# Performance work log

Hardware: AMD Instinct MI355X
Metric: run time of the kernel (lower is better)

Reference implementation:

```python
import jax, jax.numpy as jnp
import numpy as np

N_HEADS = 16
D_EMBED = 1024
D_HEAD = D_EMBED // N_HEADS
CAUSAL = True


def setup_inputs() -> dict:
    key = jax.random.key(0)
    k1, k2, k3, k4, k5 = jax.random.split(key, 5)
    B, S = 2, 2048
    scale = 1.0 / np.sqrt(D_EMBED)
    return {
        "x": jax.random.normal(k1, (B, S, D_EMBED), dtype=jnp.float32),
        "Wqkv": jax.random.normal(k2, (D_EMBED, 3 * D_EMBED), dtype=jnp.float32) * scale,
        "bqkv": jax.random.normal(k3, (3 * D_EMBED,), dtype=jnp.float32) * 0.01,
        "Wo": jax.random.normal(k4, (D_EMBED, D_EMBED), dtype=jnp.float32) * scale,
        "bo": jax.random.normal(k5, (D_EMBED,), dtype=jnp.float32) * 0.01,
    }


def reference(x, Wqkv, bqkv, Wo, bo):
    B, S, D = x.shape
    qkv = x @ Wqkv + bqkv                      # [B,S,3D]
    q, k, v = jnp.split(qkv, 3, axis=-1)
    # [B,S,D] -> [B,H,S,dh]
    def heads(t):
        return t.reshape(B, S, N_HEADS, D_HEAD).transpose(0, 2, 1, 3)
    q, k, v = heads(q), heads(k), heads(v)
    scores = jnp.einsum('bhqd,bhkd->bhqk', q, k)
    if CAUSAL:
        mask = jnp.triu(jnp.ones((S, S), dtype=bool), k=1)  # True above diagonal
        scores = jnp.where(mask, -jnp.inf, scores)
    scores = scores / jnp.sqrt(jnp.asarray(D_HEAD, dtype=scores.dtype))
    attn = jax.nn.softmax(scores, axis=-1)
    out = jnp.einsum('bhqk,bhkd->bhqd', attn, v)           # [B,H,S,dh]
    out = out.transpose(0, 2, 1, 3).reshape(B, S, D)
    return out @ Wo + bo
```

## Files before the change

kernel.cpp:

```cpp
#include <hip/hip_runtime.h>
#include <hip/hip_bf16.h>
#include <cstdint>
#include <cstddef>


using bf16 = __hip_bfloat16;
typedef __attribute__((ext_vector_type(8))) short short8;
typedef __attribute__((ext_vector_type(4))) float f32x4;
typedef __attribute__((ext_vector_type(16))) float f32x16;
typedef __attribute__((ext_vector_type(4))) unsigned int u32x4;

__device__ __forceinline__ unsigned short f2b(float f) {
    bf16 h = __float2bfloat16(f);
    return *reinterpret_cast<unsigned short*>(&h);
}

__device__ __forceinline__ void async16(const void* g, void* l) {
    __builtin_amdgcn_global_load_lds(
        (const __attribute__((address_space(1))) void*)g,
        (__attribute__((address_space(3))) void*)l, 16, 0, 0);
}

__global__ __launch_bounds__(256) void cvt_kernel(const float* __restrict__ in,
                                                  bf16* __restrict__ out, int n4) {
    int i = blockIdx.x * 256 + threadIdx.x;
    if (i >= n4) return;
    const float4 v = reinterpret_cast<const float4*>(in)[i];
    ushort4 o;
    o.x = f2b(v.x); o.y = f2b(v.y); o.z = f2b(v.z); o.w = f2b(v.w);
    reinterpret_cast<ushort4*>(out)[i] = o;
}

__global__ __launch_bounds__(256) void transpose_cvt(const float* __restrict__ in,
                                                     bf16* __restrict__ out,
                                                     int K, int N) {
    __shared__ float tile[32][33];
    int n0 = blockIdx.x * 32, k0 = blockIdx.y * 32;
    int tx = threadIdx.x, ty = threadIdx.y;
    #pragma unroll
    for (int i = 0; i < 32; i += 8)
        tile[ty + i][tx] = in[(size_t)(k0 + ty + i) * N + n0 + tx];
    __syncthreads();
    #pragma unroll
    for (int i = 0; i < 32; i += 8)
        out[(size_t)(n0 + ty + i) * K + k0 + tx] = __float2bfloat16(tile[tx][ty + i]);
}

template <int EPI>
__global__ __launch_bounds__(256) void gemm_bt64(
    const bf16* __restrict__ A,
    const bf16* __restrict__ Bt,
    const float* __restrict__ bias,
    float* __restrict__ Cf,
    bf16* __restrict__ qd, bf16* __restrict__ kd, bf16* __restrict__ vtd,
    int M, int N, int K) {
    __shared__ bf16 As[128 * 64];
    __shared__ bf16 Bs[128 * 64];
    const int t = threadIdx.x;
    const int lane = t & 63;
    const int lr = lane & 15, lg = lane >> 4;
    const int wave = t >> 6;
    const int wr = wave >> 1, wc = wave & 1;
    const int m0 = blockIdx.x * 128, n0 = blockIdx.y * 128;

    const int sRow = t >> 3;
    const int sChunk = (t & 7) ^ (sRow & 7);
    const bf16* aSrc = A + (size_t)(m0 + sRow) * K + sChunk * 8;
    const bf16* bSrc = Bt + (size_t)(n0 + sRow) * K + sChunk * 8;
    const size_t rowStep32 = (size_t)32 * K;

    f32x4 acc[4][4] = {};

    for (int k0 = 0; k0 < K; k0 += 64) {
        __syncthreads();
        #pragma unroll
        for (int j = 0; j < 4; ++j) {
            async16(aSrc + j * rowStep32 + k0, &As[j * 2048 + t * 8]);
            async16(bSrc + j * rowStep32 + k0, &Bs[j * 2048 + t * 8]);
        }
        __syncthreads();
        #pragma unroll
        for (int kh = 0; kh < 2; ++kh) {
            short8 af[4], bfr[4];
            #pragma unroll
            for (int i = 0; i < 4; ++i) {
                const int ar = wr * 64 + i * 16 + lr;
                af[i] = *reinterpret_cast<const short8*>(
                    &As[ar * 64 + ((kh * 4 + lg) ^ (ar & 7)) * 8]);
                const int br = wc * 64 + i * 16 + lr;
                bfr[i] = *reinterpret_cast<const short8*>(
                    &Bs[br * 64 + ((kh * 4 + lg) ^ (br & 7)) * 8]);
            }
            #pragma unroll
            for (int mi = 0; mi < 4; ++mi)
                #pragma unroll
                for (int ni = 0; ni < 4; ++ni)
                    acc[mi][ni] = __builtin_amdgcn_mfma_f32_16x16x32_bf16(
                        af[mi], bfr[ni], acc[mi][ni], 0, 0, 0);
        }
    }

    #pragma unroll
    for (int mi = 0; mi < 4; ++mi) {
        #pragma unroll
        for (int ni = 0; ni < 4; ++ni) {
            #pragma unroll
            for (int r = 0; r < 4; ++r) {
                const int row = m0 + wr * 64 + mi * 16 + lg * 4 + r;
                const int col = n0 + wc * 64 + ni * 16 + lr;
                const float v = acc[mi][ni][r] + bias[col];
                if constexpr (EPI == 0) {
                    Cf[(size_t)row * N + col] = v;
                } else {
                    const bf16 hv = __float2bfloat16(v);
                    const int part = col >> 10;
                    const int within = col & 1023;
                    const int h = within >> 6, d = within & 63;
                    const int b = row >> 11, s = row & 2047;
                    const int bh = b * 16 + h;
                    if (part == 0)
                        qd[((size_t)bh * 2048 + s) * 64 + d] = hv;
                    else if (part == 1)
                        kd[((size_t)bh * 2048 + s) * 64 + d] = hv;
                    else
                        vtd[((size_t)bh * 64 + d) * 2048 + s] = hv;
                }
            }
        }
    }
}

__global__ __launch_bounds__(256, 2) void attn_kernel(const bf16* __restrict__ q,
                                                      const bf16* __restrict__ k,
                                                      const bf16* __restrict__ vt,
                                                      bf16* __restrict__ o) {
    const int S = 2048;
    const int f = blockIdx.x;
    const int res = f & 7, m = f >> 3;
    const int grp = m >> 4;
    const int bh = res + 8 * grp;
    const int bxr = m & 15;
    const int bx = (grp & 2) ? (15 - bxr) : bxr;
    const int b = bh >> 4, h = bh & 15;
    const int w = threadIdx.x >> 6;
    const int u = w >> 1, par = w & 1;
    const int lane = threadIdx.x & 63;
    const int ln = lane & 31;
    const int hi = lane >> 5;
    const int P = 2 * (15 - bx) + u;
    const int qbaseA = P * 64;
    const int qbaseB = P * 64 + 32;

    const bf16* qp = q + (size_t)bh * S * 64;
    const bf16* kp = k + (size_t)bh * S * 64;
    const bf16* vp = vt + (size_t)bh * 64 * S;

    short8 qfA[4], qfB[4];
    #pragma unroll
    for (int i = 0; i < 4; ++i) {
        qfA[i] = *reinterpret_cast<const short8*>(
            &qp[(size_t)(qbaseA + ln) * 64 + i * 16 + hi * 8]);
        qfB[i] = *reinterpret_cast<const short8*>(
            &qp[(size_t)(qbaseB + ln) * 64 + i * 16 + hi * 8]);
    }

    f32x16 oA0 = {}, oA1 = {}, oB0 = {}, oB1 = {};
    f32x4 lsvA = {0.f, 0.f, 0.f, 0.f}, lsvB = {0.f, 0.f, 0.f, 0.f};

    short8 kA[4], kB[4], vA[4], vB[4];

    auto kload = [&](short8 (&kf)[4], int tile) {
        const bf16* base = &kp[(size_t)(tile * 32 + ln) * 64 + hi * 8];
        #pragma unroll
        for (int i = 0; i < 4; ++i)
            kf[i] = *reinterpret_cast<const short8*>(base + i * 16);
    };
    auto vload = [&](short8 (&vf)[4], int tile) {
        #pragma unroll
        for (int dblk = 0; dblk < 2; ++dblk)
            #pragma unroll
            for (int half = 0; half < 2; ++half)
                vf[dblk * 2 + half] = *reinterpret_cast<const short8*>(
                    &vp[(size_t)(dblk * 32 + ln) * S + tile * 32 + half * 16 +
                        hi * 8]);
    };

    auto body = [&](const short8 (&kf)[4], const short8 (&vf)[4],
                    const short8 (&qf)[4], f32x16& o0, f32x16& o1, f32x4& lsv,
                    bool diag) {
        f32x16 z0 = {}, z1 = {};
        z0 = __builtin_amdgcn_mfma_f32_32x32x16_bf16(kf[0], qf[0], z0, 0, 0, 0);
        z0 = __builtin_amdgcn_mfma_f32_32x32x16_bf16(kf[1], qf[1], z0, 0, 0, 0);
        z1 = __builtin_amdgcn_mfma_f32_32x32x16_bf16(kf[2], qf[2], z1, 0, 0, 0);
        z1 = __builtin_amdgcn_mfma_f32_32x32x16_bf16(kf[3], qf[3], z1, 0, 0, 0);
        const f32x16 z = z0 + z1;
        f32x16 pv;
        #pragma unroll
        for (int r = 0; r < 16; ++r) {
            const int kreg = (r & 3) + 8 * (r >> 2) + 4 * hi;
            float e = __expf(z[r] * 0.125f);
            if (diag && (kreg > ln)) e = 0.f;
            pv[r] = e;
            lsv[r & 3] += e;
        }
        unsigned a0, a1, b0, b1, c0, c1, d0, d1;
        asm("v_cvt_pk_bf16_f32 %0, %1, %2" : "=v"(a0) : "v"(pv[0]), "v"(pv[1]));
        asm("v_cvt_pk_bf16_f32 %0, %1, %2" : "=v"(a1) : "v"(pv[2]), "v"(pv[3]));
        asm("v_cvt_pk_bf16_f32 %0, %1, %2" : "=v"(b0) : "v"(pv[4]), "v"(pv[5]));
        asm("v_cvt_pk_bf16_f32 %0, %1, %2" : "=v"(b1) : "v"(pv[6]), "v"(pv[7]));
        asm("v_cvt_pk_bf16_f32 %0, %1, %2" : "=v"(c0) : "v"(pv[8]), "v"(pv[9]));
        asm("v_cvt_pk_bf16_f32 %0, %1, %2" : "=v"(c1) : "v"(pv[10]), "v"(pv[11]));
        asm("v_cvt_pk_bf16_f32 %0, %1, %2" : "=v"(d0) : "v"(pv[12]), "v"(pv[13]));
        asm("v_cvt_pk_bf16_f32 %0, %1, %2" : "=v"(d1) : "v"(pv[14]), "v"(pv[15]));
        asm("v_permlane32_swap_b32 %0, %1" : "+v"(a0), "+v"(b0));
        asm("v_permlane32_swap_b32 %0, %1" : "+v"(a1), "+v"(b1));
        asm("v_permlane32_swap_b32 %0, %1" : "+v"(c0), "+v"(d0));
        asm("v_permlane32_swap_b32 %0, %1" : "+v"(c1), "+v"(d1));
        u32x4 t0, t1;
        t0[0] = a0; t0[1] = a1; t0[2] = b0; t0[3] = b1;
        t1[0] = c0; t1[1] = c1; t1[2] = d0; t1[3] = d1;
        const short8 pa0 = __builtin_bit_cast(short8, t0);
        const short8 pa1 = __builtin_bit_cast(short8, t1);
        o0 = __builtin_amdgcn_mfma_f32_32x32x16_bf16(pa0, vf[0], o0, 0, 0, 0);
        o0 = __builtin_amdgcn_mfma_f32_32x32x16_bf16(pa1, vf[1], o0, 0, 0, 0);
        o1 = __builtin_amdgcn_mfma_f32_32x32x16_bf16(pa0, vf[2], o1, 0, 0, 0);
        o1 = __builtin_amdgcn_mfma_f32_32x32x16_bf16(pa1, vf[3], o1, 0, 0, 0);
    };

    auto dual = [&](const short8 (&kf)[4], const short8 (&vf)[4]) {
        body(kf, vf, qfA, oA0, oA1, lsvA, false);
        body(kf, vf, qfB, oB0, oB1, lsvB, false);
    };
    auto final_body = [&](const short8 (&kf)[4], const short8 (&vf)[4]) {
        if (par == 0) {
            body(kf, vf, qfA, oA0, oA1, lsvA, true);
            body(kf, vf, qfB, oB0, oB1, lsvB, false);
        } else {
            body(kf, vf, qfB, oB0, oB1, lsvB, true);
        }
    };

    kload(kA, par);
    vload(vA, par);
    int i = 0;
    for (; i + 2 <= P; i += 2) {
        kload(kB, par + 2 * (i + 1));
        vload(vB, par + 2 * (i + 1));
        dual(kA, vA);
        kload(kA, par + 2 * (i + 2));
        vload(vA, par + 2 * (i + 2));
        dual(kB, vB);
    }
    if (i < P) {
        kload(kB, par + 2 * P);
        vload(vB, par + 2 * P);
        dual(kA, vA);
        final_body(kB, vB);
    } else {
        final_body(kA, vA);
    }

    float lsA = (lsvA[0] + lsvA[1]) + (lsvA[2] + lsvA[3]);
    float lsB = (lsvB[0] + lsvB[1]) + (lsvB[2] + lsvB[3]);

    __shared__ float red[2][64][65];
    __shared__ float redl[2][64][2];
    if (par == 1) {
        float* dst = red[u][lane];
        #pragma unroll
        for (int r = 0; r < 16; ++r) {
            dst[r] = oA0[r];
            dst[16 + r] = oA1[r];
            dst[32 + r] = oB0[r];
            dst[48 + r] = oB1[r];
        }
        redl[u][lane][0] = lsA;
        redl[u][lane][1] = lsB;
    }
    __syncthreads();
    if (par == 1) return;
    {
        const float* src = red[u][lane];
        #pragma unroll
        for (int r = 0; r < 16; ++r) {
            oA0[r] += src[r];
            oA1[r] += src[16 + r];
            oB0[r] += src[32 + r];
            oB1[r] += src[48 + r];
        }
        lsA += redl[u][lane][0];
        lsB += redl[u][lane][1];
    }

    lsA += __shfl_xor(lsA, 32, 64);
    lsB += __shfl_xor(lsB, 32, 64);
    const float myInvA = 1.0f / lsA;
    const float myInvB = 1.0f / lsB;
    #pragma unroll
    for (int r = 0; r < 16; ++r) {
        const int qrow = (r & 3) + 8 * (r >> 2) + 4 * hi;
        const float invA = __shfl(myInvA, qrow, 64);
        const float invB = __shfl(myInvB, qrow, 64);
        const size_t rowA = ((size_t)b * S + qbaseA + qrow) * 1024 + h * 64;
        const size_t rowB = ((size_t)b * S + qbaseB + qrow) * 1024 + h * 64;
        o[rowA + ln] = __float2bfloat16(oA0[r] * invA);
        o[rowA + 32 + ln] = __float2bfloat16(oA1[r] * invA);
        o[rowB + ln] = __float2bfloat16(oB0[r] * invB);
        o[rowB + 32 + ln] = __float2bfloat16(oB1[r] * invB);
    }
}

extern "C" void kernel_launch(void* const* d_in, const int* in_sizes, int n_in,
                              void* d_out, int out_size, void* d_ws, size_t ws_size,
                              hipStream_t stream) {
    const float* x = (const float*)d_in[0];
    const float* Wqkv = (const float*)d_in[1];
    const float* bqkv = (const float*)d_in[2];
    const float* Wo = (const float*)d_in[3];
    const float* bo = (const float*)d_in[4];
    float* out = (float*)d_out;
    char* ws = (char*)d_ws;

    bf16* x_bf = (bf16*)(ws);
    bf16* wqkv_t = (bf16*)(ws + 8388608);
    bf16* wo_t = (bf16*)(ws + 14680064);
    bf16* qb = (bf16*)(ws + 16777216);
    bf16* kb = (bf16*)(ws + 25165824);
    bf16* vtb = (bf16*)(ws + 33554432);
    bf16* attn_o = x_bf;

    cvt_kernel<<<4096, 256, 0, stream>>>(x, x_bf, 1048576);
    transpose_cvt<<<dim3(96, 32), dim3(32, 8), 0, stream>>>(Wqkv, wqkv_t, 1024, 3072);
    transpose_cvt<<<dim3(32, 32), dim3(32, 8), 0, stream>>>(Wo, wo_t, 1024, 1024);
    gemm_bt64<1><<<dim3(32, 24), 256, 0, stream>>>(x_bf, wqkv_t, bqkv, nullptr,
                                                   qb, kb, vtb, 4096, 3072, 1024);
    attn_kernel<<<512, 256, 0, stream>>>(qb, kb, vtb, attn_o);
    gemm_bt64<0><<<dim3(32, 8), 256, 0, stream>>>(attn_o, wo_t, bo, out, nullptr,
                                                  nullptr, nullptr, 4096, 1024, 1024);
}
```

Before: 129.1 us.

## Fuse prep kernels, split attention over four waves, vectorize V store, narrow out-proj tile

```diff
diff --git a/kernel.cpp b/kernel.cpp
--- a/kernel.cpp
+++ b/kernel.cpp
@@ -21,22 +21,34 @@
         (__attribute__((address_space(3))) void*)l, 16, 0, 0);
 }
 
-__global__ __launch_bounds__(256) void cvt_kernel(const float* __restrict__ in,
-                                                  bf16* __restrict__ out, int n4) {
-    int i = blockIdx.x * 256 + threadIdx.x;
-    if (i >= n4) return;
-    const float4 v = reinterpret_cast<const float4*>(in)[i];
-    ushort4 o;
-    o.x = f2b(v.x); o.y = f2b(v.y); o.z = f2b(v.z); o.w = f2b(v.w);
-    reinterpret_cast<ushort4*>(out)[i] = o;
-}
-
-__global__ __launch_bounds__(256) void transpose_cvt(const float* __restrict__ in,
-                                                     bf16* __restrict__ out,
-                                                     int K, int N) {
+__global__ __launch_bounds__(256) void prep_kernel(
+    const float* __restrict__ x, bf16* __restrict__ x_bf,
+    const float* __restrict__ Wqkv, bf16* __restrict__ wqkv_t,
+    const float* __restrict__ Wo, bf16* __restrict__ wo_t) {
+    const int bid = blockIdx.x;
+    const int tid = threadIdx.x;
+    if (bid < 4096) {
+        const int i = bid * 256 + tid;
+        const float4 v = reinterpret_cast<const float4*>(x)[i];
+        ushort4 o;
+        o.x = f2b(v.x); o.y = f2b(v.y); o.z = f2b(v.z); o.w = f2b(v.w);
+        reinterpret_cast<ushort4*>(x_bf)[i] = o;
+        return;
+    }
     __shared__ float tile[32][33];
-    int n0 = blockIdx.x * 32, k0 = blockIdx.y * 32;
-    int tx = threadIdx.x, ty = threadIdx.y;
+    const float* in;
+    bf16* out;
+    int K, N, n0, k0;
+    if (bid < 4096 + 3072) {
+        const int blk = bid - 4096;
+        in = Wqkv; out = wqkv_t; K = 1024; N = 3072;
+        n0 = (blk % 96) * 32; k0 = (blk / 96) * 32;
+    } else {
+        const int blk = bid - 7168;
+        in = Wo; out = wo_t; K = 1024; N = 1024;
+        n0 = (blk % 32) * 32; k0 = (blk / 32) * 32;
+    }
+    const int tx = tid & 31, ty = tid >> 5;
     #pragma unroll
     for (int i = 0; i < 32; i += 8)
         tile[ty + i][tx] = in[(size_t)(k0 + ty + i) * N + n0 + tx];
@@ -46,7 +58,7 @@
         out[(size_t)(n0 + ty + i) * K + k0 + tx] = __float2bfloat16(tile[tx][ty + i]);
 }
 
-template <int EPI>
+template <int EPI, int BN>
 __global__ __launch_bounds__(256) void gemm_bt64(
     const bf16* __restrict__ A,
     const bf16* __restrict__ Bt,
@@ -54,14 +66,15 @@
     float* __restrict__ Cf,
     bf16* __restrict__ qd, bf16* __restrict__ kd, bf16* __restrict__ vtd,
     int M, int N, int K) {
+    constexpr int NFR = BN / 32;
     __shared__ bf16 As[128 * 64];
-    __shared__ bf16 Bs[128 * 64];
+    __shared__ bf16 Bs[BN * 64];
     const int t = threadIdx.x;
     const int lane = t & 63;
     const int lr = lane & 15, lg = lane >> 4;
     const int wave = t >> 6;
     const int wr = wave >> 1, wc = wave & 1;
-    const int m0 = blockIdx.x * 128, n0 = blockIdx.y * 128;
+    const int m0 = blockIdx.x * 128, n0 = blockIdx.y * BN;
 
     const int sRow = t >> 3;
     const int sChunk = (t & 7) ^ (sRow & 7);
@@ -69,32 +82,36 @@
     const bf16* bSrc = Bt + (size_t)(n0 + sRow) * K + sChunk * 8;
     const size_t rowStep32 = (size_t)32 * K;
 
-    f32x4 acc[4][4] = {};
+    f32x4 acc[4][NFR] = {};
 
     for (int k0 = 0; k0 < K; k0 += 64) {
         __syncthreads();
         #pragma unroll
-        for (int j = 0; j < 4; ++j) {
+        for (int j = 0; j < 4; ++j)
             async16(aSrc + j * rowStep32 + k0, &As[j * 2048 + t * 8]);
+        #pragma unroll
+        for (int j = 0; j < BN / 32; ++j)
             async16(bSrc + j * rowStep32 + k0, &Bs[j * 2048 + t * 8]);
-        }
         __syncthreads();
         #pragma unroll
         for (int kh = 0; kh < 2; ++kh) {
-            short8 af[4], bfr[4];
+            short8 af[4], bfr[NFR];
             #pragma unroll
             for (int i = 0; i < 4; ++i) {
                 const int ar = wr * 64 + i * 16 + lr;
                 af[i] = *reinterpret_cast<const short8*>(
                     &As[ar * 64 + ((kh * 4 + lg) ^ (ar & 7)) * 8]);
-                const int br = wc * 64 + i * 16 + lr;
+            }
+            #pragma unroll
+            for (int i = 0; i < NFR; ++i) {
+                const int br = wc * (BN / 2) + i * 16 + lr;
                 bfr[i] = *reinterpret_cast<const short8*>(
                     &Bs[br * 64 + ((kh * 4 + lg) ^ (br & 7)) * 8]);
             }
             #pragma unroll
             for (int mi = 0; mi < 4; ++mi)
                 #pragma unroll
-                for (int ni = 0; ni < 4; ++ni)
+                for (int ni = 0; ni < NFR; ++ni)
                     acc[mi][ni] = __builtin_amdgcn_mfma_f32_16x16x32_bf16(
                         af[mi], bfr[ni], acc[mi][ni], 0, 0, 0);
         }
@@ -103,51 +120,55 @@
     #pragma unroll
     for (int mi = 0; mi < 4; ++mi) {
         #pragma unroll
-        for (int ni = 0; ni < 4; ++ni) {
-            #pragma unroll
-            for (int r = 0; r < 4; ++r) {
-                const int row = m0 + wr * 64 + mi * 16 + lg * 4 + r;
-                const int col = n0 + wc * 64 + ni * 16 + lr;
-                const float v = acc[mi][ni][r] + bias[col];
-                if constexpr (EPI == 0) {
-                    Cf[(size_t)row * N + col] = v;
+        for (int ni = 0; ni < NFR; ++ni) {
+            const int rowb = m0 + wr * 64 + mi * 16 + lg * 4;
+            const int col = n0 + wc * (BN / 2) + ni * 16 + lr;
+            if constexpr (EPI == 0) {
+                #pragma unroll
+                for (int r = 0; r < 4; ++r)
+                    Cf[(size_t)(rowb + r) * N + col] = acc[mi][ni][r] + bias[col];
+            } else {
+                const float bs = bias[col];
+                const int part = col >> 10;
+                const int within = col & 1023;
+                const int h = within >> 6, d = within & 63;
+                const int b = rowb >> 11, s0 = rowb & 2047;
+                const int bh = b * 16 + h;
+                if (part == 2) {
+                    ushort4 pk;
+                    pk.x = f2b(acc[mi][ni][0] + bs);
+                    pk.y = f2b(acc[mi][ni][1] + bs);
+                    pk.z = f2b(acc[mi][ni][2] + bs);
+                    pk.w = f2b(acc[mi][ni][3] + bs);
+                    *reinterpret_cast<ushort4*>(
+                        &vtd[((size_t)bh * 64 + d) * 2048 + s0]) = pk;
                 } else {
-                    const bf16 hv = __float2bfloat16(v);
-                    const int part = col >> 10;
-                    const int within = col & 1023;
-                    const int h = within >> 6, d = within & 63;
-                    const int b = row >> 11, s = row & 2047;
-                    const int bh = b * 16 + h;
-                    if (part == 0)
-                        qd[((size_t)bh * 2048 + s) * 64 + d] = hv;
-                    else if (part == 1)
-                        kd[((size_t)bh * 2048 + s) * 64 + d] = hv;
-                    else
-                        vtd[((size_t)bh * 64 + d) * 2048 + s] = hv;
+                    bf16* dst = (part == 0) ? qd : kd;
+                    #pragma unroll
+                    for (int r = 0; r < 4; ++r)
+                        dst[((size_t)bh * 2048 + s0 + r) * 64 + d] =
+                            __float2bfloat16(acc[mi][ni][r] + bs);
                 }
             }
         }
     }
 }
 
-__global__ __launch_bounds__(256, 2) void attn_kernel(const bf16* __restrict__ q,
+__global__ __launch_bounds__(256, 4) void attn_kernel(const bf16* __restrict__ q,
                                                       const bf16* __restrict__ k,
                                                       const bf16* __restrict__ vt,
                                                       bf16* __restrict__ o) {
     const int S = 2048;
     const int f = blockIdx.x;
-    const int res = f & 7, m = f >> 3;
-    const int grp = m >> 4;
-    const int bh = res + 8 * grp;
-    const int bxr = m & 15;
-    const int bx = (grp & 2) ? (15 - bxr) : bxr;
+    const int r8 = f & 7, m = f >> 3;
+    const int bh = r8 + 8 * (m >> 5);
+    const int j = m & 31;
+    const int P = (j & 1) ? (j >> 1) : (31 - (j >> 1));
     const int b = bh >> 4, h = bh & 15;
     const int w = threadIdx.x >> 6;
-    const int u = w >> 1, par = w & 1;
     const int lane = threadIdx.x & 63;
     const int ln = lane & 31;
     const int hi = lane >> 5;
-    const int P = 2 * (15 - bx) + u;
     const int qbaseA = P * 64;
     const int qbaseB = P * 64 + 32;
 
@@ -196,12 +217,12 @@
         const f32x16 z = z0 + z1;
         f32x16 pv;
         #pragma unroll
-        for (int r = 0; r < 16; ++r) {
-            const int kreg = (r & 3) + 8 * (r >> 2) + 4 * hi;
-            float e = __expf(z[r] * 0.125f);
+        for (int rr = 0; rr < 16; ++rr) {
+            const int kreg = (rr & 3) + 8 * (rr >> 2) + 4 * hi;
+            float e = __expf(z[rr] * 0.125f);
             if (diag && (kreg > ln)) e = 0.f;
-            pv[r] = e;
-            lsv[r & 3] += e;
+            pv[rr] = e;
+            lsv[rr & 3] += e;
         }
         unsigned a0, a1, b0, b1, c0, c1, d0, d1;
         asm("v_cvt_pk_bf16_f32 %0, %1, %2" : "=v"(a0) : "v"(pv[0]), "v"(pv[1]));
@@ -227,86 +248,87 @@
         o1 = __builtin_amdgcn_mfma_f32_32x32x16_bf16(pa1, vf[3], o1, 0, 0, 0);
     };
 
-    auto dual = [&](const short8 (&kf)[4], const short8 (&vf)[4]) {
-        body(kf, vf, qfA, oA0, oA1, lsvA, false);
-        body(kf, vf, qfB, oB0, oB1, lsvB, false);
-    };
-    auto final_body = [&](const short8 (&kf)[4], const short8 (&vf)[4]) {
-        if (par == 0) {
-            body(kf, vf, qfA, oA0, oA1, lsvA, true);
-            body(kf, vf, qfB, oB0, oB1, lsvB, false);
+    const int tmax = 2 * P + 1;
+    const int n = (tmax >= w) ? ((tmax - w) >> 2) + 1 : 0;
+    if (n > 0) {
+        kload(kA, w);
+        vload(vA, w);
+        for (int i = 0; i + 1 < n; ++i) {
+            const int tn = w + 4 * (i + 1);
+            kload(kB, tn);
+            vload(vB, tn);
+            body(kA, vA, qfA, oA0, oA1, lsvA, false);
+            body(kA, vA, qfB, oB0, oB1, lsvB, false);
+            #pragma unroll
+            for (int c = 0; c < 4; ++c) { kA[c] = kB[c]; vA[c] = vB[c]; }
+        }
+        const int tLast = w + 4 * (n - 1);
+        if (tLast == 2 * P) {
+            body(kA, vA, qfA, oA0, oA1, lsvA, true);
+            body(kA, vA, qfB, oB0, oB1, lsvB, false);
+        } else if (tLast == tmax) {
+            body(kA, vA, qfB, oB0, oB1, lsvB, true);
         } else {
-            body(kf, vf, qfB, oB0, oB1, lsvB, true);
-        }
-    };
-
-    kload(kA, par);
-    vload(vA, par);
-    int i = 0;
-    for (; i + 2 <= P; i += 2) {
-        kload(kB, par + 2 * (i + 1));
-        vload(vB, par + 2 * (i + 1));
-        dual(kA, vA);
-        kload(kA, par + 2 * (i + 2));
-        vload(vA, par + 2 * (i + 2));
-        dual(kB, vB);
-    }
-    if (i < P) {
-        kload(kB, par + 2 * P);
-        vload(vB, par + 2 * P);
-        dual(kA, vA);
-        final_body(kB, vB);
-    } else {
-        final_body(kA, vA);
+            body(kA, vA, qfA, oA0, oA1, lsvA, false);
+            body(kA, vA, qfB, oB0, oB1, lsvB, false);
+        }
     }
 
     float lsA = (lsvA[0] + lsvA[1]) + (lsvA[2] + lsvA[3]);
     float lsB = (lsvB[0] + lsvB[1]) + (lsvB[2] + lsvB[3]);
 
-    __shared__ float red[2][64][65];
+    __shared__ float red[2][64][66];
     __shared__ float redl[2][64][2];
-    if (par == 1) {
-        float* dst = red[u][lane];
-        #pragma unroll
-        for (int r = 0; r < 16; ++r) {
-            dst[r] = oA0[r];
-            dst[16 + r] = oA1[r];
-            dst[32 + r] = oB0[r];
-            dst[48 + r] = oB1[r];
-        }
-        redl[u][lane][0] = lsA;
-        redl[u][lane][1] = lsB;
-    }
+    auto writeBuf = [&](int bi) {
+        float* dst = red[bi][lane];
+        #pragma unroll
+        for (int rr = 0; rr < 16; ++rr) {
+            dst[rr] = oA0[rr];
+            dst[16 + rr] = oA1[rr];
+            dst[32 + rr] = oB0[rr];
+            dst[48 + rr] = oB1[rr];
+        }
+        redl[bi][lane][0] = lsA;
+        redl[bi][lane][1] = lsB;
+    };
+    auto addBuf = [&](int bi) {
+        const float* src = red[bi][lane];
+        #pragma unroll
+        for (int rr = 0; rr < 16; ++rr) {
+            oA0[rr] += src[rr];
+            oA1[rr] += src[16 + rr];
+            oB0[rr] += src[32 + rr];
+            oB1[rr] += src[48 + rr];
+        }
+        lsA += redl[bi][lane][0];
+        lsB += redl[bi][lane][1];
+    };
+    if (w == 2) writeBuf(0);
+    if (w == 3) writeBuf(1);
     __syncthreads();
-    if (par == 1) return;
-    {
-        const float* src = red[u][lane];
-        #pragma unroll
-        for (int r = 0; r < 16; ++r) {
-            oA0[r] += src[r];
-            oA1[r] += src[16 + r];
-            oB0[r] += src[32 + r];
-            oB1[r] += src[48 + r];
-        }
-        lsA += redl[u][lane][0];
-        lsB += redl[u][lane][1];
-    }
+    if (w == 0) addBuf(0);
+    if (w == 1) addBuf(1);
+    __syncthreads();
+    if (w == 1) writeBuf(0);
+    __syncthreads();
+    if (w != 0) return;
+    addBuf(0);
 
     lsA += __shfl_xor(lsA, 32, 64);
     lsB += __shfl_xor(lsB, 32, 64);
     const float myInvA = 1.0f / lsA;
     const float myInvB = 1.0f / lsB;
     #pragma unroll
-    for (int r = 0; r < 16; ++r) {
-        const int qrow = (r & 3) + 8 * (r >> 2) + 4 * hi;
+    for (int rr = 0; rr < 16; ++rr) {
+        const int qrow = (rr & 3) + 8 * (rr >> 2) + 4 * hi;
         const float invA = __shfl(myInvA, qrow, 64);
         const float invB = __shfl(myInvB, qrow, 64);
         const size_t rowA = ((size_t)b * S + qbaseA + qrow) * 1024 + h * 64;
         const size_t rowB = ((size_t)b * S + qbaseB + qrow) * 1024 + h * 64;
-        o[rowA + ln] = __float2bfloat16(oA0[r] * invA);
-        o[rowA + 32 + ln] = __float2bfloat16(oA1[r] * invA);
-        o[rowB + ln] = __float2bfloat16(oB0[r] * invB);
-        o[rowB + 32 + ln] = __float2bfloat16(oB1[r] * invB);
+        o[rowA + ln] = __float2bfloat16(oA0[rr] * invA);
+        o[rowA + 32 + ln] = __float2bfloat16(oA1[rr] * invA);
+        o[rowB + ln] = __float2bfloat16(oB0[rr] * invB);
+        o[rowB + 32 + ln] = __float2bfloat16(oB1[rr] * invB);
     }
 }
 
@@ -329,12 +351,10 @@
     bf16* vtb = (bf16*)(ws + 33554432);
     bf16* attn_o = x_bf;
 
-    cvt_kernel<<<4096, 256, 0, stream>>>(x, x_bf, 1048576);
-    transpose_cvt<<<dim3(96, 32), dim3(32, 8), 0, stream>>>(Wqkv, wqkv_t, 1024, 3072);
-    transpose_cvt<<<dim3(32, 32), dim3(32, 8), 0, stream>>>(Wo, wo_t, 1024, 1024);
-    gemm_bt64<1><<<dim3(32, 24), 256, 0, stream>>>(x_bf, wqkv_t, bqkv, nullptr,
-                                                   qb, kb, vtb, 4096, 3072, 1024);
-    attn_kernel<<<512, 256, 0, stream>>>(qb, kb, vtb, attn_o);
-    gemm_bt64<0><<<dim3(32, 8), 256, 0, stream>>>(attn_o, wo_t, bo, out, nullptr,
-                                                  nullptr, nullptr, 4096, 1024, 1024);
-}
+    prep_kernel<<<8192, 256, 0, stream>>>(x, x_bf, Wqkv, wqkv_t, Wo, wo_t);
+    gemm_bt64<1, 128><<<dim3(32, 24), 256, 0, stream>>>(
+        x_bf, wqkv_t, bqkv, nullptr, qb, kb, vtb, 4096, 3072, 1024);
+    attn_kernel<<<1024, 256, 0, stream>>>(qb, kb, vtb, attn_o);
+    gemm_bt64<0, 64><<<dim3(32, 16), 256, 0, stream>>>(
+        attn_o, wo_t, bo, out, nullptr, nullptr, nullptr, 4096, 1024, 1024);
+}
```

New measurement: 512.6 us. 3.97x slower.
